# Performance work log

Measured on AMD Instinct MI355X. Metric: run time of the kernel, lower is better.

The kernel has to match this reference:

```python
import jax, jax.numpy as jnp
from jax import lax
import numpy as np

B, C, T = 128, 9, 512
M = 64                 # fourier modes
D_OB = 40
D_MODEL = C * D_OB     # 360
D_PE = 16
D = D_MODEL + D_PE     # 376
NHEAD = 4
DH = D // NHEAD        # 94
NHID = 2 * D_MODEL     # 720
NLAYERS = 3
FRAC = 0.5
MAX_PE = 100.0
EPS = 1e-5

def setup_inputs() -> dict:
    key = jax.random.key(0)
    ks = jax.random.split(key, 16)
    scale = 1.0 / (C * C)
    f32 = jnp.float32
    return {
        "x": jax.random.normal(ks[0], (B, C, T), f32),
        "w1r": scale * jax.random.uniform(ks[1], (C, C, M), f32),
        "w1i": scale * jax.random.uniform(ks[2], (C, C, M), f32),
        "conv_w": 0.1 * jax.random.normal(ks[3], (1, C, 3), f32),
        "bnf_g": jnp.ones((2 * M,), f32), "bnf_b": jnp.zeros((2 * M,), f32),
        "R_u": 1.0 + 0.02 * jax.random.normal(ks[4], (D_MODEL,), f32),
        "Wg1": 0.1 * jax.random.normal(ks[5], (D_OB, D_OB), f32),
        "Wg2": 0.1 * jax.random.normal(ks[6], (D_OB, D_OB), f32),
        "Wqkv": 0.02 * jax.random.normal(ks[7], (NLAYERS, D, 3 * D), f32),
        "bqkv": jnp.zeros((NLAYERS, 3 * D), f32),
        "Wo": 0.02 * jax.random.normal(ks[8], (NLAYERS, D, D), f32),
        "bo": jnp.zeros((NLAYERS, D), f32),
        "ln1g": jnp.ones((NLAYERS, D), f32), "ln1b": jnp.zeros((NLAYERS, D), f32),
        "W1": 0.02 * jax.random.normal(ks[9], (NLAYERS, D, NHID), f32),
        "b1": jnp.zeros((NLAYERS, NHID), f32),
        "W2": 0.02 * jax.random.normal(ks[10], (NLAYERS, NHID, D), f32),
        "b2": jnp.zeros((NLAYERS, D), f32),
        "ln2g": jnp.ones((NLAYERS, D), f32), "ln2b": jnp.zeros((NLAYERS, D), f32),
        "Wp": 0.02 * jax.random.normal(ks[11], (D, T), f32),
        "bp": jnp.zeros((T,), f32),
        "bnp_g": jnp.ones((T,), f32), "bnp_b": jnp.zeros((T,), f32),
    }

def _layernorm(z, g, b):
    m = z.mean(-1, keepdims=True)
    v = ((z - m) ** 2).mean(-1, keepdims=True)
    return (z - m) * lax.rsqrt(v + EPS) * g + b

def _batchnorm(z, g, b):  # training-mode BN over batch dim, z: [N, F]
    m = z.mean(0)
    v = ((z - m) ** 2).mean(0)
    return (z - m) * lax.rsqrt(v + EPS) * g + b

def _forward(x, w1r, w1i, conv_w, bnf_g, bnf_b, R_u, Wg1, Wg2,
             Wqkv, bqkv, Wo, bo, ln1g, ln1b, W1, b1, W2, b2, ln2g, ln2b,
             Wp, bp, bnp_g, bnp_b):
    # ---- SpectralConv1d (FrFT branch) ----
    xc = jnp.cos(x)                                   # [B,C,T]
    k = jnp.arange(T, dtype=jnp.float32)
    chirp = jnp.exp(-1j * jnp.pi * FRAC * k * k / T)  # FrFT chirp
    x_frft = jnp.fft.ifft(jnp.fft.fft(xc) * chirp)    # [B,C,T] complex
    w1 = (w1r + 1j * w1i).astype(jnp.complex64)
    out_modes = jnp.einsum('bix,iox->box', x_frft[:, :, :M], w1)   # [B,C,M]
    out_ft = jnp.concatenate([out_modes, jnp.zeros((B, C, T - M), jnp.complex64)], -1)
    ef = jnp.concatenate([jnp.abs(out_modes), jnp.angle(out_modes)], -1)  # [B,C,2M]
    # avg: Conv1d(C->1, k=3, pad=1, stride=1, no bias), then squeeze
    ef = lax.conv_general_dilated(ef, conv_w, window_strides=(1,), padding=((1, 1),),
                                  dimension_numbers=('NCH', 'OIH', 'NCH'))[:, 0, :]  # [B,2M]
    ef = jax.nn.relu(_batchnorm(ef, bnf_g, bnf_b))
    # ---- Raindrop branch ----
    src = jnp.transpose(x, (2, 0, 1))                 # [T,B,C]
    h = jnp.repeat(src, D_OB, axis=-1)                # repeat_interleave -> [T,B,d_model]
    h = jax.nn.relu(h * R_u)
    h4 = h.reshape(T, B, C, D_OB)
    adj = jnp.full((C, C), 1.0 / C, x.dtype)          # global_structure = ones, normalized
    h4 = jax.nn.relu(jnp.einsum('mn,tbnd,de->tbme', adj, h4, Wg1))
    h4 = jax.nn.relu(jnp.einsum('mn,tbnd,de->tbme', adj, h4, Wg2))
    h = h4.reshape(T, B, D_MODEL)
    # time positional encoding (PositionalEncodingTF, d_pe=16, MAX=100)
    times = jnp.broadcast_to(jnp.arange(T, dtype=jnp.float32)[:, None], (T, B))
    timescales = jnp.power(MAX_PE, jnp.linspace(0.0, 1.0, D_PE // 2))
    st = times[:, :, None] / timescales               # [T,B,8]
    pe = jnp.concatenate([jnp.sin(st), jnp.cos(st)], -1)  # [T,B,16]
    z = jnp.concatenate([h, pe], -1).transpose(1, 0, 2)   # [B,T,D]
    inv_sqrt_dh = 1.0 / np.sqrt(DH).astype(np.float32)
    for l in range(NLAYERS):
        qkv = z @ Wqkv[l] + bqkv[l]
        q, kk, v = jnp.split(qkv, 3, axis=-1)
        hd = lambda t: t.reshape(B, T, NHEAD, DH).transpose(0, 2, 1, 3)
        q, kk, v = hd(q), hd(kk), hd(v)
        att = jax.nn.softmax(jnp.einsum('bhqd,bhkd->bhqk', q, kk) * inv_sqrt_dh, axis=-1)
        o = jnp.einsum('bhqk,bhkd->bhqd', att, v).transpose(0, 2, 1, 3).reshape(B, T, D)
        z = _layernorm(z + o @ Wo[l] + bo[l], ln1g[l], ln1b[l])
        ff = jax.nn.relu(z @ W1[l] + b1[l]) @ W2[l] + b2[l]
        z = _layernorm(z + ff, ln2g[l], ln2b[l])
    et = z.mean(axis=1)                               # 'mean' aggregation -> [B,D]
    # projection: Linear(D, T) + ReLU + BatchNorm1d(T)
    et = _batchnorm(jax.nn.relu(et @ Wp + bp), bnp_g, bnp_b)  # [B,T]
    f = jnp.concatenate([ef, et], -1)                 # [B, 2M+T]
    fn = f / jnp.maximum(jnp.linalg.norm(f, axis=-1, keepdims=True), 1e-12)
    return fn, out_ft

def reference(x, w1r, w1i, conv_w, bnf_g, bnf_b, R_u, Wg1, Wg2,
              Wqkv, bqkv, Wo, bo, ln1g, ln1b, W1, b1, W2, b2, ln2g, ln2b,
              Wp, bp, bnp_g, bnp_b):
    return _forward(x, w1r, w1i, conv_w, bnf_g, bnf_b, R_u, Wg1, Wg2,
                    Wqkv, bqkv, Wo, bo, ln1g, ln1b, W1, b1, W2, b2, ln2g, ln2b,
                    Wp, bp, bnp_g, bnp_b)
```

## Files before the change

### kernel.cpp

```cpp
#include <hip/hip_runtime.h>
#include <math.h>

constexpr int cB = 128;
constexpr int cC = 9;
constexpr int cT = 512;
constexpr int cM = 64;
constexpr int cDOB = 40;
constexpr int cDM = 360;
constexpr int cD = 376;
constexpr int cDH = 94;
constexpr int cNHID = 720;
constexpr float cEPS = 1e-5f;
constexpr float cPI = 3.14159265358979323846f;

typedef __attribute__((ext_vector_type(8))) short short8b;
typedef __attribute__((ext_vector_type(4))) float f32x4;

__device__ __forceinline__ short f2b(float f) {
  union { float f; unsigned u; } c; c.f = f;
  unsigned r = (c.u + 0x7fffu + ((c.u >> 16) & 1u)) >> 16;
  return (short)r;
}
__device__ __forceinline__ float b2f(short h) {
  union { unsigned u; float f; } c; c.u = ((unsigned)(unsigned short)h) << 16;
  return c.f;
}

__global__ void k_chirp(float2* __restrict__ g) {
  int d = threadIdx.x;
  float re = 0.f, im = 0.f;
  for (int k = 0; k < cT; ++k) {
    int q = (k * k) & 2047;
    int p = (k * d) & 511;
    float th = cPI * ((float)p * (1.0f / 256.0f) - (float)q * (1.0f / 1024.0f));
    float s, c;
    sincosf(th, &s, &c);
    re += c; im += s;
  }
  g[d] = make_float2(re * (1.0f / 512.0f), im * (1.0f / 512.0f));
}

__global__ __launch_bounds__(512) void k_spectral(
    const float* __restrict__ x, const float* __restrict__ w1r,
    const float* __restrict__ w1i, const float2* __restrict__ g,
    float* __restrict__ outft, float* __restrict__ EF) {
  __shared__ float xc[cC][cT];
  __shared__ float2 gs[cT];
  __shared__ float2 xfr[cC][cM];
  int b = blockIdx.x, tid = threadIdx.x;
  for (int i = tid; i < cC * cT; i += 512)
    xc[i / cT][i % cT] = cosf(x[(size_t)b * cC * cT + i]);
  for (int i = tid; i < cT; i += 512) gs[i] = g[i];
  __syncthreads();
  for (int idx = tid; idx < cC * cM; idx += 512) {
    int c = idx / cM, m = idx % cM;
    float re = 0.f, im = 0.f;
    for (int t = 0; t < cT; ++t) {
      float xv = xc[c][t];
      float2 gv = gs[(m - t) & (cT - 1)];
      re += xv * gv.x; im += xv * gv.y;
    }
    xfr[c][m] = make_float2(re, im);
  }
  __syncthreads();
  for (int idx = tid; idx < cC * cM; idx += 512) {
    int o = idx / cM, m = idx % cM;
    float re = 0.f, im = 0.f;
    #pragma unroll
    for (int i = 0; i < cC; ++i) {
      float2 xv = xfr[i][m];
      float wr = w1r[(i * cC + o) * cM + m];
      float wi = w1i[(i * cC + o) * cM + m];
      re += xv.x * wr - xv.y * wi;
      im += xv.x * wi + xv.y * wr;
    }
    outft[(size_t)(b * cC + o) * cT + m] = re;
    EF[(b * cC + o) * (2 * cM) + m] = sqrtf(re * re + im * im);
    EF[(b * cC + o) * (2 * cM) + cM + m] = atan2f(im, re);
  }
  for (int idx = tid; idx < cC * (cT - cM); idx += 512) {
    int o = idx / (cT - cM);
    int r = idx % (cT - cM);
    outft[(size_t)(b * cC + o) * cT + cM + r] = 0.f;
  }
}

__global__ void k_convef(const float* __restrict__ EF, const float* __restrict__ cw,
                         float* __restrict__ efp) {
  int i = blockIdx.x * blockDim.x + threadIdx.x;
  if (i >= cB * 2 * cM) return;
  int b = i / (2 * cM), f = i % (2 * cM);
  float acc = 0.f;
  #pragma unroll
  for (int c = 0; c < cC; ++c) {
    const float* row = EF + (b * cC + c) * (2 * cM);
    if (f > 0) acc += row[f - 1] * cw[c * 3 + 0];
    acc += row[f] * cw[c * 3 + 1];
    if (f < 2 * cM - 1) acc += row[f + 1] * cw[c * 3 + 2];
  }
  efp[i] = acc;
}

__global__ __launch_bounds__(128) void k_bn(const float* __restrict__ in,
    const float* __restrict__ gam, const float* __restrict__ bet,
    float* __restrict__ dst, int F, int stride, int off, int reluAfter) {
  __shared__ float red[128];
  int f = blockIdx.x, bt = threadIdx.x;
  float v = in[(size_t)bt * F + f];
  red[bt] = v; __syncthreads();
  for (int s = 64; s > 0; s >>= 1) { if (bt < s) red[bt] += red[bt + s]; __syncthreads(); }
  float mean = red[0] * (1.0f / 128.0f);
  __syncthreads();
  float d = v - mean;
  red[bt] = d * d; __syncthreads();
  for (int s = 64; s > 0; s >>= 1) { if (bt < s) red[bt] += red[bt + s]; __syncthreads(); }
  float var = red[0] * (1.0f / 128.0f);
  float o = d * rsqrtf(var + cEPS) * gam[f] + bet[f];
  if (reluAfter) o = fmaxf(o, 0.f);
  dst[(size_t)bt * stride + off + f] = o;
}

__global__ __launch_bounds__(256) void k_raindrop(const float* __restrict__ x,
    const float* __restrict__ Ru, const float* __restrict__ Wg1,
    const float* __restrict__ Wg2, float* __restrict__ Z,
    short* __restrict__ Zb16, int bStart) {
  __shared__ float w1s[cDOB * cDOB], w2s[cDOB * cDOB], rus[cDM], tss[8];
  __shared__ float vsh[256][cDOB];
  int tid = threadIdx.x;
  for (int i = tid; i < cDOB * cDOB; i += 256) { w1s[i] = Wg1[i]; w2s[i] = Wg2[i]; }
  for (int i = tid; i < cDM; i += 256) rus[i] = Ru[i];
  if (tid < 8) tss[tid] = powf(100.0f, (float)tid * (1.0f / 7.0f));
  __syncthreads();
  int token0 = blockIdx.x * 256;
  int token = token0 + tid;
  int bl = token / cT, t = token % cT;
  int bg = bStart + bl;
  float s[cDOB];
  #pragma unroll
  for (int d = 0; d < cDOB; ++d) s[d] = 0.f;
  #pragma unroll
  for (int c = 0; c < cC; ++c) {
    float xv = x[((size_t)bg * cC + c) * cT + t];
    #pragma unroll
    for (int d = 0; d < cDOB; ++d) s[d] += fmaxf(xv * rus[c * cDOB + d], 0.f);
  }
  #pragma unroll
  for (int d = 0; d < cDOB; ++d) s[d] *= (1.0f / 9.0f);
  float u[cDOB];
  #pragma unroll
  for (int e = 0; e < cDOB; ++e) {
    float a = 0.f;
    #pragma unroll
    for (int d = 0; d < cDOB; ++d) a += s[d] * w1s[d * cDOB + e];
    u[e] = fmaxf(a, 0.f);
  }
  #pragma unroll
  for (int e = 0; e < cDOB; ++e) {
    float a = 0.f;
    #pragma unroll
    for (int d = 0; d < cDOB; ++d) a += u[d] * w2s[d * cDOB + e];
    vsh[tid][e] = fmaxf(a, 0.f);
  }
  __syncthreads();
  size_t zbase = (size_t)token0 * cD;
  for (int i = tid; i < 256 * cD; i += 256) {
    int tok = i / cD, col = i % cD;
    float val;
    if (col < cDM) {
      val = vsh[tok][col % cDOB];
    } else {
      int j = col - cDM;
      int tt = (token0 + tok) % cT;
      float st = (float)tt / tss[j & 7];
      val = (j < 8) ? sinf(st) : cosf(st);
    }
    Z[zbase + i] = val;
    Zb16[zbase + i] = f2b(val);
  }
}

__global__ __launch_bounds__(256) void k_cvtT(const float* __restrict__ in,
    short* __restrict__ out, int K, int N) {
  __shared__ float tile[32][33];
  int kb = blockIdx.x * 32, nb = blockIdx.y * 32;
  int tx = threadIdx.x & 31, ty = threadIdx.x >> 5;
  for (int i = ty; i < 32; i += 8) {
    int k = kb + i, n = nb + tx;
    tile[i][tx] = (k < K && n < N) ? in[(size_t)k * N + n] : 0.f;
  }
  __syncthreads();
  for (int i = ty; i < 32; i += 8) {
    int n = nb + i, k = kb + tx;
    if (n < N && k < K) out[(size_t)n * K + k] = f2b(tile[tx][i]);
  }
}

#define GEMM_CORE(EPILOGUE)                                                       \
  __shared__ short As[128][40];                                                   \
  __shared__ short Bs[128][40];                                                   \
  int tid = threadIdx.x;                                                          \
  int m0 = blockIdx.y * 128, n0 = blockIdx.x * 128;                               \
  int w = tid >> 6, l = tid & 63;                                                 \
  int wm = w >> 1, wn = w & 1;                                                    \
  int lr = l & 15, lg = l >> 4;                                                   \
  f32x4 acc[4][4];                                                                \
  _Pragma("unroll") for (int i = 0; i < 4; ++i)                                   \
    _Pragma("unroll") for (int j = 0; j < 4; ++j)                                 \
      _Pragma("unroll") for (int r = 0; r < 4; ++r) acc[i][j][r] = 0.f;           \
  int srow = tid >> 1, skq = (tid & 1) << 4;                                      \
  int nK = (Kd + 31) >> 5;                                                        \
  for (int ks = 0; ks < nK; ++ks) {                                               \
    int k0 = ks << 5;                                                             \
    {                                                                             \
      int gm = m0 + srow;                                                         \
      int gk = k0 + skq;                                                          \
      short tmp[16];                                                              \
      const short* ap = At + (size_t)gm * Kd + gk;                                \
      _Pragma("unroll") for (int c = 0; c < 2; ++c) {                             \
        if (gm < Mr && gk + c * 8 + 7 < Kd) {                                     \
          *(short8b*)&tmp[c * 8] = *(const short8b*)(ap + c * 8);                 \
        } else {                                                                  \
          _Pragma("unroll") for (int j = 0; j < 8; ++j) tmp[c * 8 + j] = (short)0;\
        }                                                                         \
      }                                                                           \
      *(short8b*)&As[srow][skq]     = *(short8b*)&tmp[0];                         \
      *(short8b*)&As[srow][skq + 8] = *(short8b*)&tmp[8];                         \
    }                                                                             \
    {                                                                             \
      int gn = n0 + srow;                                                         \
      int gk = k0 + skq;                                                          \
      short tmp[16];                                                              \
      const short* bp = Bt + (size_t)gn * Kd + gk;                                \
      _Pragma("unroll") for (int c = 0; c < 2; ++c) {                             \
        if (gn < Nc && gk + c * 8 + 7 < Kd) {                                     \
          *(short8b*)&tmp[c * 8] = *(const short8b*)(bp + c * 8);                 \
        } else {                                                                  \
          _Pragma("unroll") for (int j = 0; j < 8; ++j) tmp[c * 8 + j] = (short)0;\
        }                                                                         \
      }                                                                           \
      *(short8b*)&Bs[srow][skq]     = *(short8b*)&tmp[0];                         \
      *(short8b*)&Bs[srow][skq + 8] = *(short8b*)&tmp[8];                         \
    }                                                                             \
    __syncthreads();                                                              \
    short8b af[4], bf[4];                                                         \
    _Pragma("unroll") for (int i = 0; i < 4; ++i)                                 \
      af[i] = *(short8b*)&As[wm * 64 + i * 16 + lr][lg * 8];                      \
    _Pragma("unroll") for (int j = 0; j < 4; ++j)                                 \
      bf[j] = *(short8b*)&Bs[wn * 64 + j * 16 + lr][lg * 8];                      \
    _Pragma("unroll") for (int i = 0; i < 4; ++i)                                 \
      _Pragma("unroll") for (int j = 0; j < 4; ++j)                               \
        acc[i][j] = __builtin_amdgcn_mfma_f32_16x16x32_bf16(af[i], bf[j], acc[i][j], 0, 0, 0); \
    __syncthreads();                                                              \
  }                                                                               \
  _Pragma("unroll") for (int i = 0; i < 4; ++i)                                   \
    _Pragma("unroll") for (int j = 0; j < 4; ++j) {                               \
      int gn = n0 + wn * 64 + j * 16 + lr;                                        \
      if (gn >= Nc) continue;                                                     \
      float bv = bias ? bias[gn] : 0.f;                                           \
      int gmb = m0 + wm * 64 + i * 16 + lg * 4;                                   \
      _Pragma("unroll") for (int r = 0; r < 4; ++r) {                             \
        int gm = gmb + r;                                                         \
        if (gm >= Mr) continue;                                                   \
        float vv = acc[i][j][r] + bv;                                             \
        EPILOGUE                                                                  \
      }                                                                           \
    }

__global__ __launch_bounds__(256) void k_gemm_mfma2(
    const short* __restrict__ At, const short* __restrict__ Bt,
    const float* __restrict__ bias, float* __restrict__ Cm,
    int Mr, int Nc, int Kd, int relu) {
  GEMM_CORE({
    if (relu) vv = fmaxf(vv, 0.f);
    Cm[(size_t)gm * Nc + gn] = vv;
  })
}

__global__ __launch_bounds__(256) void k_gemm_b16(
    const short* __restrict__ At, const short* __restrict__ Bt,
    const float* __restrict__ bias, short* __restrict__ Cm,
    int Mr, int Nc, int Kd, int relu) {
  GEMM_CORE({
    if (relu) vv = fmaxf(vv, 0.f);
    Cm[(size_t)gm * Nc + gn] = f2b(vv);
  })
}

__global__ __launch_bounds__(256) void k_gemm_qkv(
    const short* __restrict__ At, const short* __restrict__ Bt,
    const float* __restrict__ bias, unsigned* __restrict__ Cp,
    int Mr, int Nc, int Kd) {
  GEMM_CORE({
    short hv = f2b(vv);
    short lv2 = f2b(vv - b2f(hv));
    Cp[(size_t)gm * Nc + gn] =
        ((unsigned)(unsigned short)hv) | (((unsigned)(unsigned short)lv2) << 16);
  })
}

__global__ __launch_bounds__(256) void k_gemm(const float* __restrict__ A,
    const float* __restrict__ Bm, const float* __restrict__ bias,
    float* __restrict__ Cm, int Mr, int Nc, int Kd, int relu) {
  __shared__ float As[16][68];
  __shared__ float Bs[16][68];
  int tid = threadIdx.x;
  int tx = tid & 15, ty = tid >> 4;
  int n0 = blockIdx.x * 64, m0 = blockIdx.y * 64;
  float acc[4][4] = {{0.f}};
  for (int k0 = 0; k0 < Kd; k0 += 16) {
    {
      int row = tid >> 2, kq = (tid & 3) << 2;
      int gm = m0 + row, gk = k0 + kq;
      float4 av = make_float4(0.f, 0.f, 0.f, 0.f);
      if (gm < Mr) {
        const float* ap = A + (size_t)gm * Kd + gk;
        if (gk + 3 < Kd) av = *(const float4*)ap;
        else {
          if (gk + 0 < Kd) av.x = ap[0];
          if (gk + 1 < Kd) av.y = ap[1];
          if (gk + 2 < Kd) av.z = ap[2];
        }
      }
      As[kq + 0][row] = av.x; As[kq + 1][row] = av.y;
      As[kq + 2][row] = av.z; As[kq + 3][row] = av.w;
    }
    {
      int kr = tid >> 4, nc = (tid & 15) << 2;
      int gk = k0 + kr, gn = n0 + nc;
      float4 bv = make_float4(0.f, 0.f, 0.f, 0.f);
      if (gk < Kd && gn < Nc) {
        const float* bp = Bm + (size_t)gk * Nc + gn;
        if (gn + 3 < Nc) bv = *(const float4*)bp;
        else {
          bv.x = bp[0];
          if (gn + 1 < Nc) bv.y = bp[1];
          if (gn + 2 < Nc) bv.z = bp[2];
        }
      }
      *(float4*)&Bs[kr][nc] = bv;
    }
    __syncthreads();
    #pragma unroll
    for (int k = 0; k < 16; ++k) {
      float4 a = *(const float4*)&As[k][ty << 2];
      float4 b = *(const float4*)&Bs[k][tx << 2];
      acc[0][0] += a.x * b.x; acc[0][1] += a.x * b.y; acc[0][2] += a.x * b.z; acc[0][3] += a.x * b.w;
      acc[1][0] += a.y * b.x; acc[1][1] += a.y * b.y; acc[1][2] += a.y * b.z; acc[1][3] += a.y * b.w;
      acc[2][0] += a.z * b.x; acc[2][1] += a.z * b.y; acc[2][2] += a.z * b.z; acc[2][3] += a.z * b.w;
      acc[3][0] += a.w * b.x; acc[3][1] += a.w * b.y; acc[3][2] += a.w * b.z; acc[3][3] += a.w * b.w;
    }
    __syncthreads();
  }
  #pragma unroll
  for (int i = 0; i < 4; ++i) {
    int gm = m0 + (ty << 2) + i;
    if (gm >= Mr) continue;
    #pragma unroll
    for (int j = 0; j < 4; ++j) {
      int gn = n0 + (tx << 2) + j;
      if (gn >= Nc) continue;
      float v = acc[i][j] + (bias ? bias[gn] : 0.f);
      if (relu) v = fmaxf(v, 0.f);
      Cm[(size_t)gm * Nc + gn] = v;
    }
  }
}

__global__ __launch_bounds__(256) void k_attn_mfma2(const unsigned* __restrict__ Qp,
    short* __restrict__ ATT16) {
  __shared__ __align__(16) char raw[12288 * 2 + 2 * 4 * 16 * 72 * 2 + 512];
  short* kv_h = (short*)raw;
  short* kv_l = (short*)(raw + 12288);
  int tid = threadIdx.x;
  int w = tid >> 6, l = tid & 63;
  int lr = l & 15, lg = l >> 4;
  short* p_h = (short*)(raw + 24576) + w * 16 * 72;
  short* p_l = (short*)(raw + 24576 + 9216) + w * 16 * 72;
  float* fs_w = (float*)(raw + 24576 + 18432) + w * 16;
  float* il_w = (float*)(raw + 24576 + 18432 + 256) + w * 16;
  int qb = blockIdx.x, h = blockIdx.y, bl = blockIdx.z;
  size_t tokBase = (size_t)bl * cT;
  const float scale = 0.103142125f;

  {
    size_t base = (tokBase + qb * 64) * 1128ull + h * cDH;
    for (int task = tid; task < 768; task += 256) {
      int oct = task >> 6, tok = task & 63;
      size_t src = base + (size_t)tok * 1128 + oct * 8;
      uint4 a = *(const uint4*)(Qp + src);
      uint4 b = *(const uint4*)(Qp + src + 4);
      unsigned p[8] = {a.x, a.y, a.z, a.w, b.x, b.y, b.z, b.w};
      short hv[8], lv[8];
      #pragma unroll
      for (int i = 0; i < 8; ++i) { hv[i] = (short)(p[i] & 0xffffu); lv[i] = (short)(p[i] >> 16); }
      if (oct == 11) { hv[6] = 0; hv[7] = 0; lv[6] = 0; lv[7] = 0; }
      int dst = (oct * 64 + (tok ^ (oct & 7))) * 8;
      *(short8b*)&kv_h[dst] = *(short8b*)hv;
      *(short8b*)&kv_l[dst] = *(short8b*)lv;
    }
  }
  __syncthreads();
  short8b qh_s[3], ql_s[3];
  #pragma unroll
  for (int s = 0; s < 3; ++s) {
    int o = s * 4 + lg;
    int src = (o * 64 + ((w * 16 + lr) ^ (o & 7))) * 8;
    qh_s[s] = *(short8b*)&kv_h[src];
    ql_s[s] = *(short8b*)&kv_l[src];
  }

  f32x4 of[6];
  #pragma unroll
  for (int f = 0; f < 6; ++f)
    #pragma unroll
    for (int r = 0; r < 4; ++r) of[f][r] = 0.f;
  float mrow[4], lrow[4];
  #pragma unroll
  for (int r = 0; r < 4; ++r) { mrow[r] = -1e30f; lrow[r] = 0.f; }

  for (int kt = 0; kt < 8; ++kt) {
    __syncthreads();
    {
      size_t base = (tokBase + kt * 64) * 1128ull + cD + h * cDH;
      for (int task = tid; task < 768; task += 256) {
        int oct = task >> 6, tok = task & 63;
        size_t src = base + (size_t)tok * 1128 + oct * 8;
        uint4 a = *(const uint4*)(Qp + src);
        uint4 b = *(const uint4*)(Qp + src + 4);
        unsigned p[8] = {a.x, a.y, a.z, a.w, b.x, b.y, b.z, b.w};
        short hv[8], lv[8];
        #pragma unroll
        for (int i = 0; i < 8; ++i) { hv[i] = (short)(p[i] & 0xffffu); lv[i] = (short)(p[i] >> 16); }
        if (oct == 11) { hv[6] = 0; hv[7] = 0; lv[6] = 0; lv[7] = 0; }
        int dst = (oct * 64 + (tok ^ (oct & 7))) * 8;
        *(short8b*)&kv_h[dst] = *(short8b*)hv;
        *(short8b*)&kv_l[dst] = *(short8b*)lv;
      }
    }
    __syncthreads();
    f32x4 sf4[4];
    #pragma unroll
    for (int j = 0; j < 4; ++j)
      #pragma unroll
      for (int r = 0; r < 4; ++r) sf4[j][r] = 0.f;
    #pragma unroll
    for (int j = 0; j < 4; ++j) {
      #pragma unroll
      for (int s = 0; s < 3; ++s) {
        int o = s * 4 + lg;
        int src = (o * 64 + ((j * 16 + lr) ^ (o & 7))) * 8;
        short8b bh = *(short8b*)&kv_h[src];
        short8b bl2 = *(short8b*)&kv_l[src];
        sf4[j] = __builtin_amdgcn_mfma_f32_16x16x32_bf16(qh_s[s], bh, sf4[j], 0, 0, 0);
        sf4[j] = __builtin_amdgcn_mfma_f32_16x16x32_bf16(ql_s[s], bh, sf4[j], 0, 0, 0);
        sf4[j] = __builtin_amdgcn_mfma_f32_16x16x32_bf16(qh_s[s], bl2, sf4[j], 0, 0, 0);
      }
    }
    float fscv[4];
    #pragma unroll
    for (int r = 0; r < 4; ++r) {
      float s0 = sf4[0][r] * scale, s1 = sf4[1][r] * scale;
      float s2 = sf4[2][r] * scale, s3 = sf4[3][r] * scale;
      float mx = fmaxf(fmaxf(s0, s1), fmaxf(s2, s3));
      for (int off = 8; off > 0; off >>= 1) mx = fmaxf(mx, __shfl_xor(mx, off, 16));
      float mnew = fmaxf(mrow[r], mx);
      float fsc = __expf(mrow[r] - mnew);
      float p0 = __expf(s0 - mnew), p1 = __expf(s1 - mnew);
      float p2 = __expf(s2 - mnew), p3 = __expf(s3 - mnew);
      float ps = p0 + p1 + p2 + p3;
      for (int off = 8; off > 0; off >>= 1) ps += __shfl_xor(ps, off, 16);
      lrow[r] = lrow[r] * fsc + ps;
      mrow[r] = mnew;
      fscv[r] = fsc;
      int row = (lg * 4 + r) * 72;
      short h0 = f2b(p0);
      p_h[row + 0 * 16 + lr] = h0; p_l[row + 0 * 16 + lr] = f2b(p0 - b2f(h0));
      short h1 = f2b(p1);
      p_h[row + 1 * 16 + lr] = h1; p_l[row + 1 * 16 + lr] = f2b(p1 - b2f(h1));
      short h2 = f2b(p2);
      p_h[row + 2 * 16 + lr] = h2; p_l[row + 2 * 16 + lr] = f2b(p2 - b2f(h2));
      short h3 = f2b(p3);
      p_h[row + 3 * 16 + lr] = h3; p_l[row + 3 * 16 + lr] = f2b(p3 - b2f(h3));
    }
    if (lr == 0) {
      #pragma unroll
      for (int r = 0; r < 4; ++r) fs_w[lg * 4 + r] = fscv[r];
    }
    __syncthreads();
    {
      size_t base = (tokBase + kt * 64) * 1128ull + 2 * cD + h * cDH;
      for (int task = tid; task < 768; task += 256) {
        int d = task % 96, t8 = task / 96;
        short hv[8], lv[8];
        if (d < cDH) {
          #pragma unroll
          for (int i = 0; i < 8; ++i) {
            unsigned p = Qp[base + (size_t)(t8 * 8 + i) * 1128 + d];
            hv[i] = (short)(p & 0xffffu); lv[i] = (short)(p >> 16);
          }
        } else {
          #pragma unroll
          for (int i = 0; i < 8; ++i) { hv[i] = 0; lv[i] = 0; }
        }
        int dst = d * 64 + ((t8 * 8) ^ ((d & 7) << 3));
        *(short8b*)&kv_h[dst] = *(short8b*)hv;
        *(short8b*)&kv_l[dst] = *(short8b*)lv;
      }
    }
    __syncthreads();
    float fs = fs_w[lr];
    #pragma unroll
    for (int f = 0; f < 6; ++f)
      #pragma unroll
      for (int r = 0; r < 4; ++r) of[f][r] *= fs;
    #pragma unroll
    for (int s = 0; s < 2; ++s) {
      int pof = lr * 72 + s * 32 + lg * 8;
      short8b ph = *(short8b*)&p_h[pof];
      short8b pl = *(short8b*)&p_l[pof];
      #pragma unroll
      for (int f = 0; f < 6; ++f) {
        int d = f * 16 + lr;
        int vof = d * 64 + ((s * 32 + lg * 8) ^ ((d & 7) << 3));
        short8b vh = *(short8b*)&kv_h[vof];
        short8b vl = *(short8b*)&kv_l[vof];
        of[f] = __builtin_amdgcn_mfma_f32_16x16x32_bf16(vh, ph, of[f], 0, 0, 0);
        of[f] = __builtin_amdgcn_mfma_f32_16x16x32_bf16(vl, ph, of[f], 0, 0, 0);
        of[f] = __builtin_amdgcn_mfma_f32_16x16x32_bf16(vh, pl, of[f], 0, 0, 0);
      }
    }
  }
  if (lr == 0) {
    #pragma unroll
    for (int r = 0; r < 4; ++r) il_w[lg * 4 + r] = 1.0f / lrow[r];
  }
  __syncthreads();
  float il = il_w[lr];
  float* obuf = (float*)raw;
  #pragma unroll
  for (int f = 0; f < 6; ++f) {
    #pragma unroll
    for (int r = 0; r < 4; ++r) {
      int d = f * 16 + lg * 4 + r;
      if (d < cDH) obuf[(w * 16 + lr) * 98 + d] = of[f][r] * il;
    }
  }
  __syncthreads();
  for (int idx = tid; idx < 64 * cDH; idx += 256) {
    int q = idx / cDH, d = idx % cDH;
    ATT16[(tokBase + qb * 64 + q) * (size_t)cD + h * cDH + d] = f2b(obuf[q * 98 + d]);
  }
}

__global__ __launch_bounds__(256) void k_addln(float* __restrict__ Z,
    const float* __restrict__ Y, const float* __restrict__ gam,
    const float* __restrict__ bet, short* __restrict__ Zb16) {
  int wid = threadIdx.x >> 6, lane = threadIdx.x & 63;
  size_t base = ((size_t)blockIdx.x * 4 + wid) * cD;
  float v[6];
  float sum = 0.f;
  #pragma unroll
  for (int j = 0; j < 6; ++j) {
    int c = lane + j * 64;
    float t = 0.f;
    if (c < cD) t = Z[base + c] + Y[base + c];
    v[j] = t; sum += t;
  }
  #pragma unroll
  for (int off = 32; off > 0; off >>= 1) sum += __shfl_xor(sum, off, 64);
  float mean = sum / (float)cD;
  float vs = 0.f;
  #pragma unroll
  for (int j = 0; j < 6; ++j) {
    int c = lane + j * 64;
    if (c < cD) { float d = v[j] - mean; vs += d * d; }
  }
  #pragma unroll
  for (int off = 32; off > 0; off >>= 1) vs += __shfl_xor(vs, off, 64);
  float inv = rsqrtf(vs / (float)cD + cEPS);
  #pragma unroll
  for (int j = 0; j < 6; ++j) {
    int c = lane + j * 64;
    if (c < cD) {
      float res = (v[j] - mean) * inv * gam[c] + bet[c];
      Z[base + c] = res;
      Zb16[base + c] = f2b(res);
    }
  }
}

__global__ __launch_bounds__(384) void k_meant(const float* __restrict__ Z,
    float* __restrict__ et, int bStart) {
  int bl = blockIdx.x, d = threadIdx.x;
  if (d >= cD) return;
  float s = 0.f;
  for (int t = 0; t < cT; ++t) s += Z[((size_t)bl * cT + t) * cD + d];
  et[(size_t)(bStart + bl) * cD + d] = s * (1.0f / 512.0f);
}

__global__ __launch_bounds__(128) void k_final(const float* __restrict__ fst,
    float* __restrict__ out) {
  __shared__ float red[128];
  int b = blockIdx.x, tid = threadIdx.x;
  float v[5]; float ss = 0.f;
  #pragma unroll
  for (int i = 0; i < 5; ++i) {
    v[i] = fst[(size_t)b * 640 + tid + i * 128];
    ss += v[i] * v[i];
  }
  red[tid] = ss; __syncthreads();
  for (int s = 64; s > 0; s >>= 1) { if (tid < s) red[tid] += red[tid + s]; __syncthreads(); }
  float inv = 1.0f / fmaxf(sqrtf(red[0]), 1e-12f);
  #pragma unroll
  for (int i = 0; i < 5; ++i) out[(size_t)b * 640 + tid + i * 128] = v[i] * inv;
}

extern "C" void kernel_launch(void* const* d_in, const int* in_sizes, int n_in,
                              void* d_out, int out_size, void* d_ws, size_t ws_size,
                              hipStream_t stream) {
  (void)in_sizes; (void)n_in; (void)out_size;
  const float* x     = (const float*)d_in[0];
  const float* w1r   = (const float*)d_in[1];
  const float* w1i   = (const float*)d_in[2];
  const float* convw = (const float*)d_in[3];
  const float* bnfg  = (const float*)d_in[4];
  const float* bnfb  = (const float*)d_in[5];
  const float* Ru    = (const float*)d_in[6];
  const float* Wg1   = (const float*)d_in[7];
  const float* Wg2   = (const float*)d_in[8];
  const float* Wqkv  = (const float*)d_in[9];
  const float* bqkv  = (const float*)d_in[10];
  const float* Wo    = (const float*)d_in[11];
  const float* bo    = (const float*)d_in[12];
  const float* ln1g  = (const float*)d_in[13];
  const float* ln1b  = (const float*)d_in[14];
  const float* W1    = (const float*)d_in[15];
  const float* b1    = (const float*)d_in[16];
  const float* W2    = (const float*)d_in[17];
  const float* b2    = (const float*)d_in[18];
  const float* ln2g  = (const float*)d_in[19];
  const float* ln2b  = (const float*)d_in[20];
  const float* Wp    = (const float*)d_in[21];
  const float* bp    = (const float*)d_in[22];
  const float* bnpg  = (const float*)d_in[23];
  const float* bnpb  = (const float*)d_in[24];

  float* W = (float*)d_ws;
  size_t wsFloats = ws_size / 4;
  float* fst = W;
  float* et  = fst + 81920;
  float* etp = et + 48128;
  float2* g  = (float2*)(etp + 65536);
  float* EF  = (float*)g + 1024;
  float* efp = EF + 147456;
  short* bfw = (short*)(efp + 16384);
  const size_t bfwFloats = 1660416;
  const size_t fixedFloats = 81920 + 48128 + 65536 + 1024 + 147456 + 16384 + bfwFloats;

  const size_t oQKV = 0;
  const size_t oWO  = oQKV + (size_t)3 * 1128 * 376;
  const size_t oW1  = oWO  + (size_t)3 * 376 * 376;
  const size_t oW2  = oW1  + (size_t)3 * 720 * 376;

  float* outF  = (float*)d_out;
  float* outft = outF + cB * 640;

  if (wsFloats < fixedFloats) return;

  int Bc = 0;
  float* chunk = nullptr;
  for (int c = 128; c >= 1; c >>= 1) {
    size_t need = (size_t)c * cT * 1880 + 64;
    if (fixedFloats + need <= wsFloats) { Bc = c; chunk = W + fixedFloats; break; }
  }
  bool haveChunk = (Bc > 0);

  if (haveChunk) {
    for (int l = 0; l < 3; ++l) {
      k_cvtT<<<dim3(12, 36), 256, 0, stream>>>(Wqkv + (size_t)l * cD * 1128,
          bfw + oQKV + (size_t)l * 1128 * 376, cD, 1128);
      k_cvtT<<<dim3(12, 12), 256, 0, stream>>>(Wo + (size_t)l * cD * cD,
          bfw + oWO + (size_t)l * 376 * 376, cD, cD);
      k_cvtT<<<dim3(12, 23), 256, 0, stream>>>(W1 + (size_t)l * cD * cNHID,
          bfw + oW1 + (size_t)l * 720 * 376, cD, cNHID);
      k_cvtT<<<dim3(23, 12), 256, 0, stream>>>(W2 + (size_t)l * cNHID * cD,
          bfw + oW2 + (size_t)l * 376 * 720, cNHID, cD);
    }

    float* Zb      = chunk;
    short* Zb16    = (short*)(Zb + (size_t)Bc * cT * cD);
    unsigned* QKVp = (unsigned*)(Zb16 + (size_t)Bc * cT * cD);
    short* ATT16   = (short*)(QKVp + (size_t)Bc * cT * 1128);
    for (int b0 = 0; b0 < cB; b0 += Bc) {
      int ntok = Bc * cT;
      int mt = (ntok + 127) / 128;
      short* Hb16  = (short*)QKVp;
      float* WoOut = (float*)(Hb16 + (size_t)ntok * 720);
      float* FF2o  = WoOut + (size_t)ntok * 376;
      k_raindrop<<<ntok / 256, 256, 0, stream>>>(x, Ru, Wg1, Wg2, Zb, Zb16, b0);
      for (int l = 0; l < 3; ++l) {
        k_gemm_qkv<<<dim3(9, mt), 256, 0, stream>>>(
            Zb16, bfw + oQKV + (size_t)l * 1128 * 376,
            bqkv + (size_t)l * 1128, QKVp, ntok, 1128, cD);
        k_attn_mfma2<<<dim3(8, 4, Bc), 256, 0, stream>>>(QKVp, ATT16);
        k_gemm_mfma2<<<dim3(3, mt), 256, 0, stream>>>(
            ATT16, bfw + oWO + (size_t)l * 376 * 376,
            bo + (size_t)l * cD, WoOut, ntok, cD, cD, 0);
        k_addln<<<ntok / 4, 256, 0, stream>>>(Zb, WoOut, ln1g + l * cD, ln1b + l * cD, Zb16);
        k_gemm_b16<<<dim3(6, mt), 256, 0, stream>>>(
            Zb16, bfw + oW1 + (size_t)l * 720 * 376,
            b1 + (size_t)l * cNHID, Hb16, ntok, cNHID, cD, 1);
        k_gemm_mfma2<<<dim3(3, mt), 256, 0, stream>>>(
            Hb16, bfw + oW2 + (size_t)l * 376 * 720,
            b2 + (size_t)l * cD, FF2o, ntok, cD, cNHID, 0);
        k_addln<<<ntok / 4, 256, 0, stream>>>(Zb, FF2o, ln2g + l * cD, ln2b + l * cD, Zb16);
      }
      k_meant<<<Bc, 384, 0, stream>>>(Zb, et, b0);
    }
    k_gemm<<<dim3(cT / 64, cB / 64), 256, 0, stream>>>(et, Wp, bp, etp, cB, cT, cD, 1);
  }

  k_chirp<<<1, 512, 0, stream>>>(g);
  k_spectral<<<cB, 512, 0, stream>>>(x, w1r, w1i, g, outft, EF);
  k_convef<<<(cB * 2 * cM + 255) / 256, 256, 0, stream>>>(EF, convw, efp);
  k_bn<<<2 * cM, 128, 0, stream>>>(efp, bnfg, bnfb, fst, 2 * cM, 640, 0, 1);

  if (haveChunk)
    k_bn<<<cT, 128, 0, stream>>>(etp, bnpg, bnpb, fst, cT, 640, 2 * cM, 0);

  k_final<<<cB, 128, 0, stream>>>(fst, outF);
}
```

Measured before the change: 3.312 ms.

## Deepen GEMM K-tile, swizzle workgroup order, and widen attention blocks to 128 queries

The shared GEMM core now stages a 64-wide K slice per iteration, with two MFMA sub-steps and a padded LDS row stride. That halves the number of barrier pairs per tile, and the workgroup index is remapped in a swizzled order to improve cache locality across blocks. The attention kernel moves to 512 threads covering 128 query rows per block, so each K/V tile loaded into LDS is reused by twice as many queries and grid size halves. In exchange it uses more LDS per block (larger GEMM tiles, roughly 62KB for attention), which lowers occupancy, and the Q load now takes two phases with extra barriers.

```diff
diff --git a/kernel.cpp b/kernel.cpp
--- a/kernel.cpp
+++ b/kernel.cpp
@@ -196,10 +196,14 @@
 }
 
 #define GEMM_CORE(EPILOGUE)                                                       \
-  __shared__ short As[128][40];                                                   \
-  __shared__ short Bs[128][40];                                                   \
+  __shared__ short As[128][72];                                                   \
+  __shared__ short Bs[128][72];                                                   \
   int tid = threadIdx.x;                                                          \
-  int m0 = blockIdx.y * 128, n0 = blockIdx.x * 128;                               \
+  int nbx = gridDim.x;                                                            \
+  int flat = blockIdx.y * nbx + blockIdx.x;                                       \
+  int nwg = nbx * gridDim.y;                                                      \
+  int swz = ((nwg & 7) == 0) ? ((flat & 7) * (nwg >> 3) + (flat >> 3)) : flat;    \
+  int m0 = (swz / nbx) * 128, n0 = (swz % nbx) * 128;                             \
   int w = tid >> 6, l = tid & 63;                                                 \
   int wm = w >> 1, wn = w & 1;                                                    \
   int lr = l & 15, lg = l >> 4;                                                   \
@@ -207,49 +211,49 @@
   _Pragma("unroll") for (int i = 0; i < 4; ++i)                                   \
     _Pragma("unroll") for (int j = 0; j < 4; ++j)                                 \
       _Pragma("unroll") for (int r = 0; r < 4; ++r) acc[i][j][r] = 0.f;           \
-  int srow = tid >> 1, skq = (tid & 1) << 4;                                      \
-  int nK = (Kd + 31) >> 5;                                                        \
+  int srow = tid >> 1, skq = (tid & 1) << 5;                                      \
+  int nK = (Kd + 63) >> 6;                                                        \
   for (int ks = 0; ks < nK; ++ks) {                                               \
-    int k0 = ks << 5;                                                             \
+    int k0 = ks << 6;                                                             \
     {                                                                             \
       int gm = m0 + srow;                                                         \
       int gk = k0 + skq;                                                          \
-      short tmp[16];                                                              \
       const short* ap = At + (size_t)gm * Kd + gk;                                \
-      _Pragma("unroll") for (int c = 0; c < 2; ++c) {                             \
+      _Pragma("unroll") for (int c = 0; c < 4; ++c) {                             \
+        short tmp[8];                                                             \
         if (gm < Mr && gk + c * 8 + 7 < Kd) {                                     \
-          *(short8b*)&tmp[c * 8] = *(const short8b*)(ap + c * 8);                 \
+          *(short8b*)tmp = *(const short8b*)(ap + c * 8);                         \
         } else {                                                                  \
-          _Pragma("unroll") for (int j = 0; j < 8; ++j) tmp[c * 8 + j] = (short)0;\
+          _Pragma("unroll") for (int j = 0; j < 8; ++j) tmp[j] = (short)0;        \
         }                                                                         \
+        *(short8b*)&As[srow][skq + c * 8] = *(short8b*)tmp;                       \
       }                                                                           \
-      *(short8b*)&As[srow][skq]     = *(short8b*)&tmp[0];                         \
-      *(short8b*)&As[srow][skq + 8] = *(short8b*)&tmp[8];                         \
     }                                                                             \
     {                                                                             \
       int gn = n0 + srow;                                                         \
       int gk = k0 + skq;                                                          \
-      short tmp[16];                                                              \
       const short* bp = Bt + (size_t)gn * Kd + gk;                                \
-      _Pragma("unroll") for (int c = 0; c < 2; ++c) {                             \
+      _Pragma("unroll") for (int c = 0; c < 4; ++c) {                             \
+        short tmp[8];                                                             \
         if (gn < Nc && gk + c * 8 + 7 < Kd) {                                     \
-          *(short8b*)&tmp[c * 8] = *(const short8b*)(bp + c * 8);                 \
+          *(short8b*)tmp = *(const short8b*)(bp + c * 8);                         \
         } else {                                                                  \
-          _Pragma("unroll") for (int j = 0; j < 8; ++j) tmp[c * 8 + j] = (short)0;\
+          _Pragma("unroll") for (int j = 0; j < 8; ++j) tmp[j] = (short)0;        \
         }                                                                         \
+        *(short8b*)&Bs[srow][skq + c * 8] = *(short8b*)tmp;                       \
       }                                                                           \
-      *(short8b*)&Bs[srow][skq]     = *(short8b*)&tmp[0];                         \
-      *(short8b*)&Bs[srow][skq + 8] = *(short8b*)&tmp[8];                         \
     }                                                                             \
     __syncthreads();                                                              \
-    short8b af[4], bf[4];                                                         \
-    _Pragma("unroll") for (int i = 0; i < 4; ++i)                                 \
-      af[i] = *(short8b*)&As[wm * 64 + i * 16 + lr][lg * 8];                      \
-    _Pragma("unroll") for (int j = 0; j < 4; ++j)                                 \
-      bf[j] = *(short8b*)&Bs[wn * 64 + j * 16 + lr][lg * 8];                      \
-    _Pragma("unroll") for (int i = 0; i < 4; ++i)                                 \
+    _Pragma("unroll") for (int kh = 0; kh < 2; ++kh) {                            \
+      short8b af[4], bf[4];                                                       \
+      _Pragma("unroll") for (int i = 0; i < 4; ++i)                               \
+        af[i] = *(short8b*)&As[wm * 64 + i * 16 + lr][kh * 32 + lg * 8];          \
       _Pragma("unroll") for (int j = 0; j < 4; ++j)                               \
-        acc[i][j] = __builtin_amdgcn_mfma_f32_16x16x32_bf16(af[i], bf[j], acc[i][j], 0, 0, 0); \
+        bf[j] = *(short8b*)&Bs[wn * 64 + j * 16 + lr][kh * 32 + lg * 8];          \
+      _Pragma("unroll") for (int i = 0; i < 4; ++i)                               \
+        _Pragma("unroll") for (int j = 0; j < 4; ++j)                             \
+          acc[i][j] = __builtin_amdgcn_mfma_f32_16x16x32_bf16(af[i], bf[j], acc[i][j], 0, 0, 0); \
+    }                                                                             \
     __syncthreads();                                                              \
   }                                                                               \
   _Pragma("unroll") for (int i = 0; i < 4; ++i)                                   \
@@ -366,25 +370,28 @@
   }
 }
 
-__global__ __launch_bounds__(256) void k_attn_mfma2(const unsigned* __restrict__ Qp,
+__global__ __launch_bounds__(512) void k_attn_mfma2(const unsigned* __restrict__ Qp,
     short* __restrict__ ATT16) {
-  __shared__ __align__(16) char raw[12288 * 2 + 2 * 4 * 16 * 72 * 2 + 512];
+  __shared__ __align__(16) char raw[62464];
   short* kv_h = (short*)raw;
   short* kv_l = (short*)(raw + 12288);
   int tid = threadIdx.x;
   int w = tid >> 6, l = tid & 63;
   int lr = l & 15, lg = l >> 4;
   short* p_h = (short*)(raw + 24576) + w * 16 * 72;
-  short* p_l = (short*)(raw + 24576 + 9216) + w * 16 * 72;
-  float* fs_w = (float*)(raw + 24576 + 18432) + w * 16;
-  float* il_w = (float*)(raw + 24576 + 18432 + 256) + w * 16;
+  short* p_l = (short*)(raw + 43008) + w * 16 * 72;
+  float* fs_w = (float*)(raw + 61440) + w * 16;
+  float* il_w = (float*)(raw + 61952) + w * 16;
   int qb = blockIdx.x, h = blockIdx.y, bl = blockIdx.z;
   size_t tokBase = (size_t)bl * cT;
   const float scale = 0.103142125f;
-
-  {
-    size_t base = (tokBase + qb * 64) * 1128ull + h * cDH;
-    for (int task = tid; task < 768; task += 256) {
+  int qrow = w * 16 + lr;
+
+  short8b qh_s[3], ql_s[3];
+  #pragma unroll
+  for (int ph = 0; ph < 2; ++ph) {
+    size_t base = (tokBase + qb * 128 + ph * 64) * 1128ull + h * cDH;
+    for (int task = tid; task < 768; task += 512) {
       int oct = task >> 6, tok = task & 63;
       size_t src = base + (size_t)tok * 1128 + oct * 8;
       uint4 a = *(const uint4*)(Qp + src);
@@ -398,15 +405,18 @@
       *(short8b*)&kv_h[dst] = *(short8b*)hv;
       *(short8b*)&kv_l[dst] = *(short8b*)lv;
     }
-  }
-  __syncthreads();
-  short8b qh_s[3], ql_s[3];
-  #pragma unroll
-  for (int s = 0; s < 3; ++s) {
-    int o = s * 4 + lg;
-    int src = (o * 64 + ((w * 16 + lr) ^ (o & 7))) * 8;
-    qh_s[s] = *(short8b*)&kv_h[src];
-    ql_s[s] = *(short8b*)&kv_l[src];
+    __syncthreads();
+    if ((w >> 2) == ph) {
+      int tokl = qrow & 63;
+      #pragma unroll
+      for (int s = 0; s < 3; ++s) {
+        int o = s * 4 + lg;
+        int src = (o * 64 + (tokl ^ (o & 7))) * 8;
+        qh_s[s] = *(short8b*)&kv_h[src];
+        ql_s[s] = *(short8b*)&kv_l[src];
+      }
+    }
+    __syncthreads();
   }
 
   f32x4 of[6];
@@ -422,7 +432,7 @@
     __syncthreads();
     {
       size_t base = (tokBase + kt * 64) * 1128ull + cD + h * cDH;
-      for (int task = tid; task < 768; task += 256) {
+      for (int task = tid; task < 768; task += 512) {
         int oct = task >> 6, tok = task & 63;
         size_t src = base + (size_t)tok * 1128 + oct * 8;
         uint4 a = *(const uint4*)(Qp + src);
@@ -489,7 +499,7 @@
     __syncthreads();
     {
       size_t base = (tokBase + kt * 64) * 1128ull + 2 * cD + h * cDH;
-      for (int task = tid; task < 768; task += 256) {
+      for (int task = tid; task < 768; task += 512) {
         int d = task % 96, t8 = task / 96;
         short hv[8], lv[8];
         if (d < cDH) {
@@ -546,9 +556,9 @@
     }
   }
   __syncthreads();
-  for (int idx = tid; idx < 64 * cDH; idx += 256) {
+  for (int idx = tid; idx < 128 * cDH; idx += 512) {
     int q = idx / cDH, d = idx % cDH;
-    ATT16[(tokBase + qb * 64 + q) * (size_t)cD + h * cDH + d] = f2b(obuf[q * 98 + d]);
+    ATT16[(tokBase + qb * 128 + q) * (size_t)cD + h * cDH + d] = f2b(obuf[q * 98 + d]);
   }
 }
 
@@ -702,7 +712,7 @@
         k_gemm_qkv<<<dim3(9, mt), 256, 0, stream>>>(
             Zb16, bfw + oQKV + (size_t)l * 1128 * 376,
             bqkv + (size_t)l * 1128, QKVp, ntok, 1128, cD);
-        k_attn_mfma2<<<dim3(8, 4, Bc), 256, 0, stream>>>(QKVp, ATT16);
+        k_attn_mfma2<<<dim3(4, 4, Bc), 512, 0, stream>>>(QKVp, ATT16);
         k_gemm_mfma2<<<dim3(3, mt), 256, 0, stream>>>(
             ATT16, bfw + oWO + (size_t)l * 376 * 376,
             bo + (size_t)l * cD, WoOut, ntok, cD, cD, 0);
```

After: 3.423 ms. 3.3% more time.
